# Optimization experiments

Hardware: AMD Instinct MI355X
Metric: run time of the kernel (lower is better)

The kernel has to match this reference:

```python
import jax, jax.numpy as jnp
import numpy as np

NHEAD = 16
D_MODEL = 1024
HEAD_DIM = D_MODEL // NHEAD


def setup_inputs() -> dict:
    key = jax.random.key(0)
    k1, k2, k3 = jax.random.split(key, 3)
    x = jax.random.normal(k1, (4, 2048, D_MODEL), dtype=jnp.float32)
    # lecun_normal-like scaling for stability
    w_qkv = jax.random.normal(k2, (D_MODEL, 3 * D_MODEL), dtype=jnp.float32) / np.sqrt(D_MODEL)
    w_out = jax.random.normal(k3, (D_MODEL, D_MODEL), dtype=jnp.float32) / np.sqrt(D_MODEL)
    return {"x": x, "w_qkv": w_qkv, "w_out": w_out}


def reference(x, w_qkv, w_out):
    # Fused QKV projection (self-attention: x_kv = x)
    qkv = x @ w_qkv  # [B, S, 3*D]
    q, k, v = jnp.split(qkv, 3, axis=-1)
    B, S = x.shape[0], x.shape[1]
    # [B, S, H, hd] -> [B, H, S, hd]
    q = jnp.moveaxis(q.reshape(B, S, NHEAD, HEAD_DIM), -2, -3)
    k = jnp.moveaxis(k.reshape(B, S, NHEAD, HEAD_DIM), -2, -3)
    v = jnp.moveaxis(v.reshape(B, S, NHEAD, HEAD_DIM), -2, -3)
    scale = 1.0 / jnp.sqrt(jnp.float32(HEAD_DIM))
    logits = jnp.einsum('bhqd,bhkd->bhqk', q, k) * scale
    weights = jax.nn.softmax(logits, axis=-1)
    out = jnp.einsum('bhqk,bhkd->bhqd', weights, v)  # [B, H, S, hd]
    out = jnp.moveaxis(out, -3, -2).reshape(B, S, D_MODEL)
    return out @ w_out
```

## Files before the change

kernel.cpp:

```cpp
#include <hip/hip_runtime.h>
#include <hip/hip_bf16.h>
#include <math.h>

#define D_MODEL 1024
#define NHEAD   16
#define HEAD_DIM 64
#define BATCH   4
#define SEQ     2048

typedef __attribute__((ext_vector_type(8))) short bf16x8;
typedef __attribute__((ext_vector_type(4))) float f32x4;
typedef __attribute__((ext_vector_type(16))) float f32x16;

__device__ inline ushort f2bf(float f) {
  __hip_bfloat16 h = __float2bfloat16(f);
  return *reinterpret_cast<ushort*>(&h);
}
__device__ inline uint pk2(float a, float b) {
  return (uint)f2bf(a) | ((uint)f2bf(b) << 16);
}
__device__ inline float bf2f(ushort u) {
  return __uint_as_float((uint)u << 16);
}
__device__ inline f32x16 zero16() {
  f32x16 z;
#pragma unroll
  for (int i = 0; i < 16; ++i) z[i] = 0.f;
  return z;
}
__device__ inline float fexp2(float x) { return __builtin_amdgcn_exp2f(x); }

__device__ inline void gld_lds16(const ushort* g, ushort* l) {
  __builtin_amdgcn_global_load_lds(
      (const __attribute__((address_space(1))) void*)g,
      (__attribute__((address_space(3))) void*)l, 16, 0, 0);
}

__global__ __launch_bounds__(256) void fill_f32(float* __restrict__ p, int n, float v) {
  int i = blockIdx.x * 256 + threadIdx.x;
  if (i < n) p[i] = v;
}

__global__ __launch_bounds__(256) void cast_bf16(const float* __restrict__ in,
                                                 ushort* __restrict__ out, int n8) {
  int i = blockIdx.x * 256 + threadIdx.x;
  if (i >= n8) return;
  const float4* p = (const float4*)(in + i * 8);
  float4 a = p[0], b = p[1];
  uint4 o;
  o.x = pk2(a.x, a.y); o.y = pk2(a.z, a.w);
  o.z = pk2(b.x, b.y); o.w = pk2(b.z, b.w);
  ((uint4*)out)[i] = o;
}

__global__ __launch_bounds__(256) void transpose_f32_bf16(const float* __restrict__ in,
                                                          ushort* __restrict__ out,
                                                          int R, int C) {
  __shared__ float tile[32][33];
  int tx = threadIdx.x, ty = threadIdx.y;
  int c0 = blockIdx.x * 32, r0 = blockIdx.y * 32;
#pragma unroll
  for (int k = 0; k < 4; ++k)
    tile[ty + 8 * k][tx] = in[(size_t)(r0 + ty + 8 * k) * C + c0 + tx];
  __syncthreads();
#pragma unroll
  for (int k = 0; k < 4; ++k)
    out[(size_t)(c0 + ty + 8 * k) * R + r0 + tx] = f2bf(tile[tx][ty + 8 * k]);
}

__device__ inline bf16x8 lds_read_swz(const ushort* base, int byteoff) {
  byteoff ^= ((byteoff >> 7) & 7) << 4;
  return *(const bf16x8*)((const char*)base + byteoff);
}

template <typename OutT>
__global__ __launch_bounds__(512, 2) void gemm_mfma256(const ushort* __restrict__ A,
                                                       const ushort* __restrict__ BT,
                                                       OutT* __restrict__ C,
                                                       int M, int N, int K) {
  __shared__ ushort AS[2][256 * 64];
  __shared__ ushort BS[2][128 * 64];

  const int tid = threadIdx.x;
  const int w = tid >> 6, lane = tid & 63;
  const int quad = lane >> 4, l16 = lane & 15;
  const int wm = w >> 2, wn = w & 3;

  int bx = blockIdx.x, by = blockIdx.y;
  {
    int nwg = gridDim.x * gridDim.y;
    if ((nwg & 7) == 0) {
      int bid = by * gridDim.x + bx;
      int chunk = nwg >> 3;
      bid = (bid & 7) * chunk + (bid >> 3);
      bx = bid % gridDim.x;
      by = bid / gridDim.x;
    }
  }
  const int m0 = by * 256, n0 = bx * 128;

  f32x4 acc[8][2];
#pragma unroll
  for (int mt = 0; mt < 8; ++mt)
#pragma unroll
    for (int nt = 0; nt < 2; ++nt) acc[mt][nt] = (f32x4){0.f, 0.f, 0.f, 0.f};

  const ushort* asrc[4];
  const ushort* bsrc[2];
  uint adst[4], bdst[2];
#pragma unroll
  for (int i = 0; i < 4; ++i) {
    int x = (i * 512 + tid) * 16;
    int sx = x ^ (((x >> 7) & 7) << 4);
    asrc[i] = A + (size_t)(m0 + (sx >> 7)) * K + ((sx & 127) >> 1);
    adst[i] = (uint)(i * 512 + w * 64) * 8;
  }
#pragma unroll
  for (int i = 0; i < 2; ++i) {
    int x = (i * 512 + tid) * 16;
    int sx = x ^ (((x >> 7) & 7) << 4);
    bsrc[i] = BT + (size_t)(n0 + (sx >> 7)) * K + ((sx & 127) >> 1);
    bdst[i] = (uint)(i * 512 + w * 64) * 8;
  }

  const int NKT = K >> 6;

#pragma unroll
  for (int i = 0; i < 4; ++i) gld_lds16(asrc[i], AS[0] + adst[i]);
#pragma unroll
  for (int i = 0; i < 2; ++i) gld_lds16(bsrc[i], BS[0] + bdst[i]);

  for (int kt = 0; kt < NKT; ++kt) {
    const int cur = kt & 1;

    asm volatile("s_waitcnt vmcnt(0)" ::: "memory");
    __builtin_amdgcn_s_barrier();

    if (kt + 1 < NKT) {
      const int k0n = (kt + 1) << 6;
#pragma unroll
      for (int i = 0; i < 4; ++i) gld_lds16(asrc[i] + k0n, AS[cur ^ 1] + adst[i]);
#pragma unroll
      for (int i = 0; i < 2; ++i) gld_lds16(bsrc[i] + k0n, BS[cur ^ 1] + bdst[i]);
    }

    bf16x8 bfr[2][2], af[4][2];
#pragma unroll
    for (int fn = 0; fn < 2; ++fn)
#pragma unroll
      for (int kk = 0; kk < 2; ++kk)
        bfr[fn][kk] = lds_read_swz(BS[cur], (wn * 32 + fn * 16 + l16) * 128 + kk * 64 + quad * 16);
#pragma unroll
    for (int f = 0; f < 4; ++f)
#pragma unroll
      for (int kk = 0; kk < 2; ++kk)
        af[f][kk] = lds_read_swz(AS[cur], (wm * 128 + f * 16 + l16) * 128 + kk * 64 + quad * 16);
    __builtin_amdgcn_s_setprio(1);
#pragma unroll
    for (int f = 0; f < 4; ++f)
#pragma unroll
      for (int fn = 0; fn < 2; ++fn)
#pragma unroll
        for (int kk = 0; kk < 2; ++kk)
          acc[f][fn] = __builtin_amdgcn_mfma_f32_16x16x32_bf16(af[f][kk], bfr[fn][kk], acc[f][fn], 0, 0, 0);
    __builtin_amdgcn_s_setprio(0);
#pragma unroll
    for (int f = 0; f < 4; ++f)
#pragma unroll
      for (int kk = 0; kk < 2; ++kk)
        af[f][kk] = lds_read_swz(AS[cur], (wm * 128 + 64 + f * 16 + l16) * 128 + kk * 64 + quad * 16);
    __builtin_amdgcn_s_setprio(1);
#pragma unroll
    for (int f = 0; f < 4; ++f)
#pragma unroll
      for (int fn = 0; fn < 2; ++fn)
#pragma unroll
        for (int kk = 0; kk < 2; ++kk)
          acc[4 + f][fn] = __builtin_amdgcn_mfma_f32_16x16x32_bf16(af[f][kk], bfr[fn][kk], acc[4 + f][fn], 0, 0, 0);
    __builtin_amdgcn_s_setprio(0);
  }

#pragma unroll
  for (int mt = 0; mt < 8; ++mt) {
#pragma unroll
    for (int nt = 0; nt < 2; ++nt) {
#pragma unroll
      for (int r = 0; r < 4; ++r) {
        size_t idx = (size_t)(m0 + wm * 128 + mt * 16 + quad * 4 + r) * N + n0 + wn * 32 + nt * 16 + l16;
        if constexpr (sizeof(OutT) == 4) C[idx] = acc[mt][nt][r];
        else                             C[idx] = f2bf(acc[mt][nt][r]);
      }
    }
  }
}

#define KST 72
#define VST 72
#define NT  (SEQ / 64)
__global__ __launch_bounds__(256, 4) void attn_mfma(const ushort* __restrict__ qkv,
                                                    ushort* __restrict__ attn_o) {
  __shared__ ushort Ks[2][64 * KST];
  __shared__ ushort VTs[2][64 * VST];

  const int tid = threadIdx.x;
  const int w = tid >> 6, lane = tid & 63;
  const int q32 = lane & 31, hi = lane >> 5;

  const int f = blockIdx.x;
  const int xcd = f & 7;
  const int j = f >> 3;
  const int qb = j & 15;
  const int hb = ((j >> 4) << 3) | xcd;
  const int h = hb & 15, b = hb >> 4;
  const int q0 = qb * 128;

  const float qscale = 0.125f * 1.44269504088896f;
  bf16x8 qfrag[4];
  {
    const ushort* qrow = qkv + (size_t)(b * SEQ + q0 + w * 32 + q32) * 3072 + h * 64;
#pragma unroll
    for (int dd = 0; dd < 4; ++dd) {
      bf16x8 fq = *(const bf16x8*)(qrow + dd * 16 + hi * 8);
#pragma unroll
      for (int jj = 0; jj < 8; ++jj)
        fq[jj] = (short)f2bf(bf2f((ushort)fq[jj]) * qscale);
      qfrag[dd] = fq;
    }
  }

  f32x16 oacc0 = zero16(), oacc1 = zero16(), lacc = zero16();

  bf16x8 ones;
#pragma unroll
  for (int jj = 0; jj < 8; ++jj) ones[jj] = (short)0x3F80;

  const int sr = tid >> 2, sc = tid & 3;
  const int kp = tid & 31, dg = tid >> 5;

  const size_t kstep = (size_t)64 * 3072;
  const ushort* kbase = qkv + (size_t)(b * SEQ + sr) * 3072 + 1024 + h * 64 + sc * 16;
  const ushort* vbase = qkv + (size_t)(b * SEQ + 2 * kp) * 3072 + 2048 + h * 64 + dg * 8;

  uint4 kreg0, kreg1, vreg0, vreg1;
  {
    const uint4* ks = (const uint4*)kbase;
    kreg0 = ks[0]; kreg1 = ks[1];
    vreg0 = *(const uint4*)vbase;
    vreg1 = *(const uint4*)(vbase + 3072);
    uint4* kdst = (uint4*)(Ks[0] + sr * KST + sc * 16);
    kdst[0] = kreg0; kdst[1] = kreg1;
    const ushort* ae = (const ushort*)&vreg0;
    const ushort* ce = (const ushort*)&vreg1;
#pragma unroll
    for (int jj = 0; jj < 8; ++jj) {
      VTs[0][(dg * 8 + jj) * VST + 2 * kp]     = ae[jj];
      VTs[0][(dg * 8 + jj) * VST + 2 * kp + 1] = ce[jj];
    }
  }

  for (int kt = 0; kt < NT; ++kt) {
    const int cur = kt & 1;
    __syncthreads();

    if (kt + 1 < NT) {
      const uint4* ks = (const uint4*)(kbase + (size_t)(kt + 1) * kstep);
      kreg0 = ks[0]; kreg1 = ks[1];
      vreg0 = *(const uint4*)(vbase + (size_t)(kt + 1) * kstep);
      vreg1 = *(const uint4*)(vbase + (size_t)(kt + 1) * kstep + 3072);
    }

    f32x16 sacc0 = zero16(), sacc1 = zero16();
    __builtin_amdgcn_s_setprio(1);
#pragma unroll
    for (int dd = 0; dd < 4; ++dd) {
      bf16x8 kf0 = *(const bf16x8*)(Ks[cur] + (q32)*KST + dd * 16 + hi * 8);
      bf16x8 kf1 = *(const bf16x8*)(Ks[cur] + (32 + q32) * KST + dd * 16 + hi * 8);
      sacc0 = __builtin_amdgcn_mfma_f32_32x32x16_bf16(kf0, qfrag[dd], sacc0, 0, 0, 0);
      sacc1 = __builtin_amdgcn_mfma_f32_32x32x16_bf16(kf1, qfrag[dd], sacc1, 0, 0, 0);
    }
    __builtin_amdgcn_s_setprio(0);

    bf16x8 pa[4];
#pragma unroll
    for (int kblk = 0; kblk < 2; ++kblk) {
      const f32x16& sacc = kblk ? sacc1 : sacc0;
      uint d0[4], d1[4];
#pragma unroll
      for (int p = 0; p < 4; ++p) {
        d0[p] = pk2(fexp2(sacc[4 * p + 0]), fexp2(sacc[4 * p + 1]));
        d1[p] = pk2(fexp2(sacc[4 * p + 2]), fexp2(sacc[4 * p + 3]));
      }
#pragma unroll
      for (int k2 = 0; k2 < 2; ++k2) {
        uint A0 = d0[2 * k2], B0 = d0[2 * k2 + 1];
        uint A1 = d1[2 * k2], B1 = d1[2 * k2 + 1];
        asm("v_permlane32_swap_b32 %0, %1" : "+v"(A0), "+v"(B0));
        asm("v_permlane32_swap_b32 %0, %1" : "+v"(A1), "+v"(B1));
        uint4 fr = {A0, A1, B0, B1};
        pa[kblk * 2 + k2] = *(bf16x8*)&fr;
        lacc = __builtin_amdgcn_mfma_f32_32x32x16_bf16(pa[kblk * 2 + k2], ones, lacc, 0, 0, 0);
      }
    }

    __builtin_amdgcn_s_setprio(1);
#pragma unroll
    for (int kb2 = 0; kb2 < 4; ++kb2) {
      bf16x8 vf0 = *(const bf16x8*)(VTs[cur] + (q32)*VST + kb2 * 16 + hi * 8);
      bf16x8 vf1 = *(const bf16x8*)(VTs[cur] + (32 + q32) * VST + kb2 * 16 + hi * 8);
      oacc0 = __builtin_amdgcn_mfma_f32_32x32x16_bf16(pa[kb2], vf0, oacc0, 0, 0, 0);
      oacc1 = __builtin_amdgcn_mfma_f32_32x32x16_bf16(pa[kb2], vf1, oacc1, 0, 0, 0);
    }
    __builtin_amdgcn_s_setprio(0);

    if (kt + 1 < NT) {
      uint4* kdst = (uint4*)(Ks[cur ^ 1] + sr * KST + sc * 16);
      kdst[0] = kreg0; kdst[1] = kreg1;
      const ushort* ae = (const ushort*)&vreg0;
      const ushort* ce = (const ushort*)&vreg1;
#pragma unroll
      for (int jj = 0; jj < 8; ++jj) {
        VTs[cur ^ 1][(dg * 8 + jj) * VST + 2 * kp]     = ae[jj];
        VTs[cur ^ 1][(dg * 8 + jj) * VST + 2 * kp + 1] = ce[jj];
      }
    }
  }

#pragma unroll
  for (int p = 0; p < 4; ++p) {
#pragma unroll
    for (int r = 0; r < 4; ++r) {
      int qrow = r + 8 * p + 4 * hi;
      float linv = 1.0f / lacc[4 * p + r];
      ushort* orow = attn_o + (size_t)(b * SEQ + q0 + w * 32 + qrow) * 1024 + h * 64 + q32;
      orow[0]  = f2bf(oacc0[4 * p + r] * linv);
      orow[32] = f2bf(oacc1[4 * p + r] * linv);
    }
  }
}

extern "C" void kernel_launch(void* const* d_in, const int* in_sizes, int n_in,
                              void* d_out, int out_size, void* d_ws, size_t ws_size,
                              hipStream_t stream) {
  bool ok_n  = (n_in == 3);
  bool ok_s0 = ok_n && (in_sizes[0] == 4 * 2048 * 1024);
  bool ok_s1 = ok_n && (in_sizes[1] == 1024 * 3072);
  bool ok_s2 = ok_n && (in_sizes[2] == 1024 * 1024);
  bool ok_o  = (out_size == 4 * 2048 * 1024);
  bool ok_w  = (ws_size >= (size_t)8192 * 3072 * 4);
  if (!(ok_n && ok_s0 && ok_s1 && ok_s2 && ok_o && ok_w)) {
    float c = 64.0f + 1.0f * ok_n + 2.0f * ok_s0 + 4.0f * ok_s1 +
              8.0f * ok_s2 + 16.0f * ok_o + 32.0f * ok_w;
    fill_f32<<<(out_size + 255) / 256, 256, 0, stream>>>((float*)d_out, out_size, c);
    return;
  }

  const float* x     = (const float*)d_in[0];
  const float* w_qkv = (const float*)d_in[1];
  const float* w_out = (const float*)d_in[2];

  char* ws = (char*)d_ws;
  ushort* qkv    = (ushort*)ws;
  ushort* xb     = (ushort*)(ws + (size_t)48 * 1024 * 1024);
  ushort* attn_o = (ushort*)(ws + (size_t)64 * 1024 * 1024);
  ushort* wqkvT  = (ushort*)(ws + (size_t)80 * 1024 * 1024);
  ushort* woutT  = (ushort*)(ws + (size_t)86 * 1024 * 1024);

  cast_bf16<<<dim3(8192 * 1024 / 8 / 256), dim3(256), 0, stream>>>(x, xb, 8192 * 1024 / 8);
  transpose_f32_bf16<<<dim3(3072 / 32, 1024 / 32), dim3(32, 8), 0, stream>>>(w_qkv, wqkvT, 1024, 3072);
  transpose_f32_bf16<<<dim3(1024 / 32, 1024 / 32), dim3(32, 8), 0, stream>>>(w_out, woutT, 1024, 1024);

  gemm_mfma256<ushort><<<dim3(3072 / 128, 8192 / 256), dim3(512), 0, stream>>>(
      xb, wqkvT, qkv, 8192, 3072, 1024);

  attn_mfma<<<dim3(1024), dim3(256), 0, stream>>>(qkv, attn_o);

  gemm_mfma256<float><<<dim3(1024 / 128, 8192 / 256), dim3(512), 0, stream>>>(
      attn_o, woutT, (float*)d_out, 8192, 1024, 1024);
}
```

Baseline: 286.3 us.

## Rewrite GEMM as persistent 256x256-tile kernel with two-stage prefetch pipeline

Replaces the 256x128-tile GEMM with a 256x256-tile variant that doubles per-wave output (8x4 accumulator fragments) to raise operand reuse. It launches a persistent grid that loops over output tiles and prefetches two k-steps ahead, waiting on partial vmcnt so loads overlap the MFMA phases. The price is more LDS and registers per block, an extra barrier per k-step, and the loss of the previous block-index swizzle. The output projection now runs on only 128 blocks, which may underfill the device.

```diff
diff --git a/kernel.cpp b/kernel.cpp
--- a/kernel.cpp
+++ b/kernel.cpp
@@ -74,121 +74,145 @@
 }
 
 template <typename OutT>
-__global__ __launch_bounds__(512, 2) void gemm_mfma256(const ushort* __restrict__ A,
-                                                       const ushort* __restrict__ BT,
-                                                       OutT* __restrict__ C,
-                                                       int M, int N, int K) {
+__global__ __launch_bounds__(512, 2) void gemm_8ph(const ushort* __restrict__ A,
+                                                   const ushort* __restrict__ BT,
+                                                   OutT* __restrict__ C,
+                                                   int M, int N, int K, int n_tiles) {
   __shared__ ushort AS[2][256 * 64];
-  __shared__ ushort BS[2][128 * 64];
+  __shared__ ushort BS[2][256 * 64];
 
   const int tid = threadIdx.x;
   const int w = tid >> 6, lane = tid & 63;
   const int quad = lane >> 4, l16 = lane & 15;
   const int wm = w >> 2, wn = w & 3;
-
-  int bx = blockIdx.x, by = blockIdx.y;
-  {
-    int nwg = gridDim.x * gridDim.y;
-    if ((nwg & 7) == 0) {
-      int bid = by * gridDim.x + bx;
-      int chunk = nwg >> 3;
-      bid = (bid & 7) * chunk + (bid >> 3);
-      bx = bid % gridDim.x;
-      by = bid / gridDim.x;
-    }
-  }
-  const int m0 = by * 256, n0 = bx * 128;
-
-  f32x4 acc[8][2];
-#pragma unroll
-  for (int mt = 0; mt < 8; ++mt)
-#pragma unroll
-    for (int nt = 0; nt < 2; ++nt) acc[mt][nt] = (f32x4){0.f, 0.f, 0.f, 0.f};
-
-  const ushort* asrc[4];
-  const ushort* bsrc[2];
-  uint adst[4], bdst[2];
+  const int tiles_x = N >> 8;
+  const int NKT = K >> 6;
+
+  int arow[4], acol[4];
+  uint sdst[4];
 #pragma unroll
   for (int i = 0; i < 4; ++i) {
     int x = (i * 512 + tid) * 16;
     int sx = x ^ (((x >> 7) & 7) << 4);
-    asrc[i] = A + (size_t)(m0 + (sx >> 7)) * K + ((sx & 127) >> 1);
-    adst[i] = (uint)(i * 512 + w * 64) * 8;
-  }
-#pragma unroll
-  for (int i = 0; i < 2; ++i) {
-    int x = (i * 512 + tid) * 16;
-    int sx = x ^ (((x >> 7) & 7) << 4);
-    bsrc[i] = BT + (size_t)(n0 + (sx >> 7)) * K + ((sx & 127) >> 1);
-    bdst[i] = (uint)(i * 512 + w * 64) * 8;
-  }
-
-  const int NKT = K >> 6;
-
-#pragma unroll
-  for (int i = 0; i < 4; ++i) gld_lds16(asrc[i], AS[0] + adst[i]);
-#pragma unroll
-  for (int i = 0; i < 2; ++i) gld_lds16(bsrc[i], BS[0] + bdst[i]);
-
-  for (int kt = 0; kt < NKT; ++kt) {
-    const int cur = kt & 1;
-
-    asm volatile("s_waitcnt vmcnt(0)" ::: "memory");
-    __builtin_amdgcn_s_barrier();
-
-    if (kt + 1 < NKT) {
-      const int k0n = (kt + 1) << 6;
-#pragma unroll
-      for (int i = 0; i < 4; ++i) gld_lds16(asrc[i] + k0n, AS[cur ^ 1] + adst[i]);
-#pragma unroll
-      for (int i = 0; i < 2; ++i) gld_lds16(bsrc[i] + k0n, BS[cur ^ 1] + bdst[i]);
-    }
-
-    bf16x8 bfr[2][2], af[4][2];
-#pragma unroll
-    for (int fn = 0; fn < 2; ++fn)
-#pragma unroll
-      for (int kk = 0; kk < 2; ++kk)
-        bfr[fn][kk] = lds_read_swz(BS[cur], (wn * 32 + fn * 16 + l16) * 128 + kk * 64 + quad * 16);
-#pragma unroll
-    for (int f = 0; f < 4; ++f)
-#pragma unroll
-      for (int kk = 0; kk < 2; ++kk)
-        af[f][kk] = lds_read_swz(AS[cur], (wm * 128 + f * 16 + l16) * 128 + kk * 64 + quad * 16);
-    __builtin_amdgcn_s_setprio(1);
-#pragma unroll
-    for (int f = 0; f < 4; ++f)
-#pragma unroll
-      for (int fn = 0; fn < 2; ++fn)
+    arow[i] = sx >> 7;
+    acol[i] = (sx & 127) >> 1;
+    sdst[i] = (uint)(i * 512 + w * 64) * 8;
+  }
+
+  for (int t = blockIdx.x; t < n_tiles; t += gridDim.x) {
+    const int m0 = (t / tiles_x) << 8, n0 = (t % tiles_x) << 8;
+
+    int aoff[4], boff[4];
+#pragma unroll
+    for (int i = 0; i < 4; ++i) {
+      aoff[i] = (m0 + arow[i]) * K + acol[i];
+      boff[i] = (n0 + arow[i]) * K + acol[i];
+    }
+
+    f32x4 acc[8][4];
+#pragma unroll
+    for (int mt = 0; mt < 8; ++mt)
+#pragma unroll
+      for (int nt = 0; nt < 4; ++nt) acc[mt][nt] = (f32x4){0.f, 0.f, 0.f, 0.f};
+
+#pragma unroll
+    for (int i = 0; i < 4; ++i) gld_lds16(A + aoff[i], AS[0] + sdst[i]);
+#pragma unroll
+    for (int i = 0; i < 4; ++i) gld_lds16(BT + boff[i], BS[0] + sdst[i]);
+#pragma unroll
+    for (int i = 0; i < 4; ++i) gld_lds16(A + aoff[i] + 64, AS[1] + sdst[i]);
+#pragma unroll
+    for (int i = 0; i < 4; ++i) gld_lds16(BT + boff[i] + 64, BS[1] + sdst[i]);
+
+    for (int kt = 0; kt < NKT; ++kt) {
+      const int cur = kt & 1;
+
+      if (kt + 1 < NKT) asm volatile("s_waitcnt vmcnt(8)" ::: "memory");
+      else              asm volatile("s_waitcnt vmcnt(0)" ::: "memory");
+      __builtin_amdgcn_s_barrier();
+
+      bf16x8 af0[4][2], af1[4][2], bf0[2][2], bf1[2][2];
+
+#pragma unroll
+      for (int f = 0; f < 4; ++f)
 #pragma unroll
         for (int kk = 0; kk < 2; ++kk)
-          acc[f][fn] = __builtin_amdgcn_mfma_f32_16x16x32_bf16(af[f][kk], bfr[fn][kk], acc[f][fn], 0, 0, 0);
-    __builtin_amdgcn_s_setprio(0);
-#pragma unroll
-    for (int f = 0; f < 4; ++f)
-#pragma unroll
-      for (int kk = 0; kk < 2; ++kk)
-        af[f][kk] = lds_read_swz(AS[cur], (wm * 128 + 64 + f * 16 + l16) * 128 + kk * 64 + quad * 16);
-    __builtin_amdgcn_s_setprio(1);
-#pragma unroll
-    for (int f = 0; f < 4; ++f)
-#pragma unroll
-      for (int fn = 0; fn < 2; ++fn)
+          af0[f][kk] = lds_read_swz(AS[cur], (wm * 128 + f * 16 + l16) * 128 + kk * 64 + quad * 16);
+#pragma unroll
+      for (int g = 0; g < 2; ++g)
 #pragma unroll
         for (int kk = 0; kk < 2; ++kk)
-          acc[4 + f][fn] = __builtin_amdgcn_mfma_f32_16x16x32_bf16(af[f][kk], bfr[fn][kk], acc[4 + f][fn], 0, 0, 0);
-    __builtin_amdgcn_s_setprio(0);
-  }
-
-#pragma unroll
-  for (int mt = 0; mt < 8; ++mt) {
-#pragma unroll
-    for (int nt = 0; nt < 2; ++nt) {
-#pragma unroll
-      for (int r = 0; r < 4; ++r) {
-        size_t idx = (size_t)(m0 + wm * 128 + mt * 16 + quad * 4 + r) * N + n0 + wn * 32 + nt * 16 + l16;
-        if constexpr (sizeof(OutT) == 4) C[idx] = acc[mt][nt][r];
-        else                             C[idx] = f2bf(acc[mt][nt][r]);
+          bf0[g][kk] = lds_read_swz(BS[cur], (wn * 64 + g * 16 + l16) * 128 + kk * 64 + quad * 16);
+      __builtin_amdgcn_s_setprio(1);
+#pragma unroll
+      for (int f = 0; f < 4; ++f)
+#pragma unroll
+        for (int g = 0; g < 2; ++g)
+#pragma unroll
+          for (int kk = 0; kk < 2; ++kk)
+            acc[f][g] = __builtin_amdgcn_mfma_f32_16x16x32_bf16(af0[f][kk], bf0[g][kk], acc[f][g], 0, 0, 0);
+      __builtin_amdgcn_s_setprio(0);
+
+#pragma unroll
+      for (int f = 0; f < 4; ++f)
+#pragma unroll
+        for (int kk = 0; kk < 2; ++kk)
+          af1[f][kk] = lds_read_swz(AS[cur], (wm * 128 + 64 + f * 16 + l16) * 128 + kk * 64 + quad * 16);
+      __builtin_amdgcn_s_setprio(1);
+#pragma unroll
+      for (int f = 0; f < 4; ++f)
+#pragma unroll
+        for (int g = 0; g < 2; ++g)
+#pragma unroll
+          for (int kk = 0; kk < 2; ++kk)
+            acc[4 + f][g] = __builtin_amdgcn_mfma_f32_16x16x32_bf16(af1[f][kk], bf0[g][kk], acc[4 + f][g], 0, 0, 0);
+      __builtin_amdgcn_s_setprio(0);
+
+#pragma unroll
+      for (int g = 0; g < 2; ++g)
+#pragma unroll
+        for (int kk = 0; kk < 2; ++kk)
+          bf1[g][kk] = lds_read_swz(BS[cur], (wn * 64 + 32 + g * 16 + l16) * 128 + kk * 64 + quad * 16);
+      __builtin_amdgcn_s_setprio(1);
+#pragma unroll
+      for (int f = 0; f < 4; ++f)
+#pragma unroll
+        for (int g = 0; g < 2; ++g)
+#pragma unroll
+          for (int kk = 0; kk < 2; ++kk)
+            acc[f][2 + g] = __builtin_amdgcn_mfma_f32_16x16x32_bf16(af0[f][kk], bf1[g][kk], acc[f][2 + g], 0, 0, 0);
+      __builtin_amdgcn_s_setprio(0);
+      __builtin_amdgcn_s_barrier();
+
+      if (kt + 2 < NKT) {
+        const int k0n = (kt + 2) << 6;
+#pragma unroll
+        for (int i = 0; i < 4; ++i) gld_lds16(A + aoff[i] + k0n, AS[cur] + sdst[i]);
+#pragma unroll
+        for (int i = 0; i < 4; ++i) gld_lds16(BT + boff[i] + k0n, BS[cur] + sdst[i]);
+      }
+      __builtin_amdgcn_s_setprio(1);
+#pragma unroll
+      for (int f = 0; f < 4; ++f)
+#pragma unroll
+        for (int g = 0; g < 2; ++g)
+#pragma unroll
+          for (int kk = 0; kk < 2; ++kk)
+            acc[4 + f][2 + g] = __builtin_amdgcn_mfma_f32_16x16x32_bf16(af1[f][kk], bf1[g][kk], acc[4 + f][2 + g], 0, 0, 0);
+      __builtin_amdgcn_s_setprio(0);
+    }
+
+#pragma unroll
+    for (int mt = 0; mt < 8; ++mt) {
+#pragma unroll
+      for (int nt = 0; nt < 4; ++nt) {
+#pragma unroll
+        for (int r = 0; r < 4; ++r) {
+          size_t idx = (size_t)(m0 + wm * 128 + mt * 16 + quad * 4 + r) * N
+                       + n0 + wn * 64 + nt * 16 + l16;
+          if constexpr (sizeof(OutT) == 4) C[idx] = acc[mt][nt][r];
+          else                             C[idx] = f2bf(acc[mt][nt][r]);
+        }
       }
     }
   }
@@ -369,11 +393,11 @@
   transpose_f32_bf16<<<dim3(3072 / 32, 1024 / 32), dim3(32, 8), 0, stream>>>(w_qkv, wqkvT, 1024, 3072);
   transpose_f32_bf16<<<dim3(1024 / 32, 1024 / 32), dim3(32, 8), 0, stream>>>(w_out, woutT, 1024, 1024);
 
-  gemm_mfma256<ushort><<<dim3(3072 / 128, 8192 / 256), dim3(512), 0, stream>>>(
-      xb, wqkvT, qkv, 8192, 3072, 1024);
+  gemm_8ph<ushort><<<dim3(192), dim3(512), 0, stream>>>(
+      xb, wqkvT, qkv, 8192, 3072, 1024, 384);
 
   attn_mfma<<<dim3(1024), dim3(256), 0, stream>>>(qkv, attn_o);
 
-  gemm_mfma256<float><<<dim3(1024 / 128, 8192 / 256), dim3(512), 0, stream>>>(
-      attn_o, woutT, (float*)d_out, 8192, 1024, 1024);
-}
+  gemm_8ph<float><<<dim3(128), dim3(512), 0, stream>>>(
+      attn_o, woutT, (float*)d_out, 8192, 1024, 1024, 128);
+}
```

New measurement: 278.7 us. 1.03x faster.
